# Optimization experiments

Hardware: AMD Instinct MI355X
Metric: run time of the kernel (lower is better)

Reference implementation:

```python
import jax, jax.numpy as jnp
import numpy as np

N_NODES = 50000
N_EDGES = 800000
D_IN = 128
D_OUT = 128


def setup_inputs() -> dict:
    key = jax.random.key(0)
    ks = jax.random.split(key, 10)
    x = jax.random.normal(ks[0], (N_NODES, D_IN), dtype=jnp.float32)
    src = jax.random.randint(ks[1], (N_EDGES,), 0, N_NODES, dtype=jnp.int32)
    dst = jax.random.randint(ks[2], (N_EDGES,), 0, N_NODES, dtype=jnp.int32)
    s = 1.0 / np.sqrt(D_IN)
    def lin(k, din, dout):
        kw, kb = jax.random.split(k)
        W = jax.random.uniform(kw, (din, dout), minval=-s, maxval=s, dtype=jnp.float32)
        b = jax.random.uniform(kb, (dout,), minval=-s, maxval=s, dtype=jnp.float32)
        return W, b
    W1, b1 = lin(ks[3], D_IN, D_IN)
    W2, b2 = lin(ks[4], D_IN, D_IN)
    W3, b3 = lin(ks[5], D_IN, D_OUT)
    return dict(x=x, W1=W1, b1=b1, W2=W2, b2=b2, W3=W3, b3=b3, src=src, dst=dst)


def reference(x, W1, b1, W2, b2, W3, b3, src, dst):
    n = x.shape[0]
    ones = jnp.ones(src.shape[0], dtype=x.dtype)
    in_deg = jax.ops.segment_sum(ones, dst, num_segments=n)    # [N]
    out_deg = jax.ops.segment_sum(ones, src, num_segments=n)   # [N]

    def sage_gcn(h, W, b):
        # DGL SAGEConv(aggregator_type='gcn'), eval mode (feat_drop = identity):
        # h_neigh = (sum_{j in N(i)} h_j + h_i) / (in_deg_i + 1); out = h_neigh @ W + b
        neigh = jax.ops.segment_sum(h[src], dst, num_segments=n)  # [N, D]
        h_neigh = (neigh + h) / (in_deg + 1.0)[:, None]
        return h_neigh @ W + b

    h = sage_gcn(x, W1, b1)
    h = sage_gcn(h, W2, b2)

    # DGL GraphConv norm='both', allow_zero_in_degree=True:
    # out = D_in^{-1/2} A D_out^{-1/2} h W + b, degrees clamped to >= 1
    norm_out = jnp.clip(out_deg, 1.0) ** -0.5
    norm_in = jnp.clip(in_deg, 1.0) ** -0.5
    hs = h * norm_out[:, None]
    agg = jax.ops.segment_sum(hs[src], dst, num_segments=n)
    out = (agg * norm_in[:, None]) @ W3 + b3
    return out
```

## Files before the change

### kernel.cpp

```cpp
#include <hip/hip_runtime.h>

#define NN 50000
#define NE 800000
#define D 128

#define CH 64
#define EPC (NE / CH)
#define RG 8
#define NPR (NN / RG)

typedef short bf16x8 __attribute__((ext_vector_type(8)));
typedef float f32x4 __attribute__((ext_vector_type(4)));


__device__ __forceinline__ unsigned bf16rne(float f) {
  unsigned u = __float_as_uint(f);
  return (u + 0x7fffu + ((u >> 16) & 1u)) >> 16;
}
__device__ __forceinline__ unsigned packbf(float lo, float hi) {
  return bf16rne(lo) | (bf16rne(hi) << 16);
}

__global__ __launch_bounds__(256) void cvt_kernel(const float* __restrict__ x,
                                                  unsigned short* __restrict__ xb, int n4) {
  int i = blockIdx.x * 256 + threadIdx.x;
  if (i < n4) {
    float4 v = ((const float4*)x)[i];
    uint2 p;
    p.x = packbf(v.x, v.y);
    p.y = packbf(v.z, v.w);
    ((uint2*)xb)[i] = p;
  }
}

__global__ __launch_bounds__(256) void wcvt_kernel(const float* __restrict__ W1,
                                                   const float* __restrict__ W2,
                                                   const float* __restrict__ W3,
                                                   unsigned short* __restrict__ T1,
                                                   unsigned short* __restrict__ T2,
                                                   unsigned short* __restrict__ T3) {
  int w = blockIdx.x >> 6;
  int i = (blockIdx.x & 63) * 256 + threadIdx.x;
  const float* W = (w == 0) ? W1 : (w == 1) ? W2 : W3;
  unsigned short* T = (w == 0) ? T1 : (w == 1) ? T2 : T3;
  int n = i >> 7, k = i & 127;
  T[n * 128 + k] = (unsigned short)bf16rne(W[k * 128 + n]);
}

__global__ __launch_bounds__(1024) void hist_kernel(const int* __restrict__ src,
                                                    const int* __restrict__ dst,
                                                    int* __restrict__ partial_dst,
                                                    int* __restrict__ partial_src) {
  __shared__ int hd[NPR];
  __shared__ int hs[NPR];
  int tid = threadIdx.x;
  int c = blockIdx.x >> 3;
  int r = blockIdx.x & 7;
  int base = r * NPR;
  for (int i = tid; i < NPR; i += 1024) { hd[i] = 0; hs[i] = 0; }
  __syncthreads();
  int e0 = c * EPC;
  for (int i = tid; i < EPC; i += 1024) {
    int d = dst[e0 + i];
    int s = src[e0 + i];
    unsigned dr = (unsigned)(d - base);
    unsigned sr = (unsigned)(s - base);
    if (dr < NPR) atomicAdd(&hd[dr], 1);
    if (sr < NPR) atomicAdd(&hs[sr], 1);
  }
  __syncthreads();
  for (int i = tid; i < NPR; i += 1024) {
    partial_dst[c * NN + base + i] = hd[i];
    partial_src[c * NN + base + i] = hs[i];
  }
}

__global__ __launch_bounds__(256) void reduce_kernel(int* __restrict__ partial_dst,
                                                     const int* __restrict__ partial_src,
                                                     int* __restrict__ degtmp,
                                                     int* __restrict__ deg_out, int N) {
  int d = blockIdx.x * 256 + threadIdx.x;
  if (d >= N) return;
  int run = 0;
#pragma unroll
  for (int c = 0; c < CH; ++c) {
    int v = partial_dst[c * NN + d];
    partial_dst[c * NN + d] = run;
    run += v;
  }
  degtmp[d] = run;
  int ro = 0;
#pragma unroll
  for (int c = 0; c < CH; ++c) ro += partial_src[c * NN + d];
  deg_out[d] = ro;
}


__device__ __forceinline__ int block_excl_scan(int v, int* wsum) {
  int lane = threadIdx.x & 63;
  int w = threadIdx.x >> 6;
  int incl = v;
#pragma unroll
  for (int off = 1; off < 64; off <<= 1) {
    int t = __shfl_up(incl, off);
    if (lane >= off) incl += t;
  }
  if (lane == 63) wsum[w] = incl;
  __syncthreads();
  int wo = 0;
#pragma unroll
  for (int j = 0; j < 4; ++j)
    if (j < w) wo += wsum[j];
  return wo + incl - v;
}

__global__ __launch_bounds__(256) void scan1(const int* __restrict__ deg,
                                             int* __restrict__ partials, int N) {
  __shared__ int wsum[4];
  int i = blockIdx.x * 256 + threadIdx.x;
  int v = (i < N) ? deg[i] : 0;
  int excl = block_excl_scan(v, wsum);
  if (threadIdx.x == 255) partials[blockIdx.x] = excl + v;
}

__global__ __launch_bounds__(256) void scan2(int* __restrict__ partials, int nb) {
  __shared__ int wsum[4];
  int v = (threadIdx.x < nb) ? partials[threadIdx.x] : 0;
  int excl = block_excl_scan(v, wsum);
  if (threadIdx.x < nb) partials[threadIdx.x] = excl;
}

__global__ __launch_bounds__(256) void scan3(const int* __restrict__ deg,
                                             const int* __restrict__ partials,
                                             int* __restrict__ row_ptr, int N) {
  __shared__ int wsum[4];
  int i = blockIdx.x * 256 + threadIdx.x;
  int v = (i < N) ? deg[i] : 0;
  int excl = block_excl_scan(v, wsum);
  if (i < N) row_ptr[i] = partials[blockIdx.x] + excl;
  if (blockIdx.x == gridDim.x - 1 && threadIdx.x == 0) row_ptr[N] = NE;
}

__global__ __launch_bounds__(1024) void fill_kernel(const int* __restrict__ src,
                                                    const int* __restrict__ dst,
                                                    const int* __restrict__ row_ptr,
                                                    const int* __restrict__ partial_dst,
                                                    int* __restrict__ csr_src) {
  __shared__ int cur[NPR];
  int tid = threadIdx.x;
  int c = blockIdx.x >> 3;
  int r = blockIdx.x & 7;
  int base = r * NPR;
  for (int i = tid; i < NPR; i += 1024)
    cur[i] = row_ptr[base + i] + partial_dst[c * NN + base + i];
  __syncthreads();
  int e0 = c * EPC;
  for (int i = tid; i < EPC; i += 1024) {
    int d = dst[e0 + i];
    unsigned dr = (unsigned)(d - base);
    if (dr < NPR) {
      int pos = atomicAdd(&cur[dr], 1);
      csr_src[pos] = src[e0 + i];
    }
  }
}

__device__ __forceinline__ void bacc(float* a, uint4 u) {
  a[0] += __uint_as_float(u.x << 16);
  a[1] += __uint_as_float(u.x & 0xffff0000u);
  a[2] += __uint_as_float(u.y << 16);
  a[3] += __uint_as_float(u.y & 0xffff0000u);
  a[4] += __uint_as_float(u.z << 16);
  a[5] += __uint_as_float(u.z & 0xffff0000u);
  a[6] += __uint_as_float(u.w << 16);
  a[7] += __uint_as_float(u.w & 0xffff0000u);
}

template <int MODE>
__global__ __launch_bounds__(256) void agg_kernel(const unsigned short* __restrict__ hb,
                                                  const int* __restrict__ row_ptr,
                                                  const int* __restrict__ csr_src,
                                                  unsigned short* __restrict__ outb, int N) {
  int wid = blockIdx.x * 4 + (threadIdx.x >> 6);
  int lane = threadIdx.x & 63;
  if (wid >= N) return;
  int start = row_ptr[wid];
  int end = row_ptr[wid + 1];
  int q = lane >> 4;
  int col = lane & 15;
  float a0[8] = {0, 0, 0, 0, 0, 0, 0, 0};
  float a1[8] = {0, 0, 0, 0, 0, 0, 0, 0};
  float a2[8] = {0, 0, 0, 0, 0, 0, 0, 0};
  float a3[8] = {0, 0, 0, 0, 0, 0, 0, 0};
  int e = start;
  for (; e + 16 <= end; e += 16) {
    int i0 = csr_src[e + q];
    int i1 = csr_src[e + 4 + q];
    int i2 = csr_src[e + 8 + q];
    int i3 = csr_src[e + 12 + q];
    uint4 u0 = ((const uint4*)(hb + (size_t)i0 * D))[col];
    uint4 u1 = ((const uint4*)(hb + (size_t)i1 * D))[col];
    uint4 u2 = ((const uint4*)(hb + (size_t)i2 * D))[col];
    uint4 u3 = ((const uint4*)(hb + (size_t)i3 * D))[col];
    bacc(a0, u0);
    bacc(a1, u1);
    bacc(a2, u2);
    bacc(a3, u3);
  }
  for (; e + 4 <= end; e += 4) {
    int i0 = csr_src[e + q];
    uint4 u0 = ((const uint4*)(hb + (size_t)i0 * D))[col];
    bacc(a0, u0);
  }
  if (q < end - e) {
    int i0 = csr_src[e + q];
    uint4 u0 = ((const uint4*)(hb + (size_t)i0 * D))[col];
    bacc(a0, u0);
  }
#pragma unroll
  for (int j = 0; j < 8; ++j) a0[j] = (a0[j] + a1[j]) + (a2[j] + a3[j]);
#pragma unroll
  for (int j = 0; j < 8; ++j) {
    a0[j] += __shfl_xor(a0[j], 16);
    a0[j] += __shfl_xor(a0[j], 32);
  }
  int indeg = end - start;
  if (MODE == 0) {
    uint4 s = ((const uint4*)(hb + (size_t)wid * D))[col];
    float sf[8] = {0, 0, 0, 0, 0, 0, 0, 0};
    bacc(sf, s);
    float inv = 1.0f / (float)(indeg + 1);
#pragma unroll
    for (int j = 0; j < 8; ++j) a0[j] = (a0[j] + sf[j]) * inv;
  } else {
    float sc = rsqrtf(fmaxf((float)indeg, 1.0f));
#pragma unroll
    for (int j = 0; j < 8; ++j) a0[j] *= sc;
  }
  if (q == 0) {
    uint4 p;
    p.x = packbf(a0[0], a0[1]);
    p.y = packbf(a0[2], a0[3]);
    p.z = packbf(a0[4], a0[5]);
    p.w = packbf(a0[6], a0[7]);
    ((uint4*)(outb + (size_t)wid * D))[col] = p;
  }
}

template <int MODE, int OUT_BF>
__global__ __launch_bounds__(256) void mgemm_kernel(const unsigned short* __restrict__ A,
                                                    const unsigned short* __restrict__ WT,
                                                    const float* __restrict__ bias,
                                                    const int* __restrict__ deg_out,
                                                    float* __restrict__ outf,
                                                    unsigned short* __restrict__ outb, int N) {
  __shared__ unsigned short sWT[128 * 136];
  int tid = threadIdx.x;
  for (int g = tid; g < 2048; g += 256) {
    int n = g >> 4, c = g & 15;
    uint4 v = ((const uint4*)WT)[g];
    *(uint4*)&sWT[n * 136 + c * 8] = v;
  }
  int wv = tid >> 6;
  int lane = tid & 63;
  int q = lane >> 4;
  int ln = lane & 15;
  int row0 = blockIdx.x * 64 + wv * 16;
  int arow = row0 + ln;
  if (arow >= N) arow = 0;
  const unsigned short* Ar = A + (size_t)arow * 128 + q * 8;
  bf16x8 af0 = *(const bf16x8*)(Ar + 0);
  bf16x8 af1 = *(const bf16x8*)(Ar + 32);
  bf16x8 af2 = *(const bf16x8*)(Ar + 64);
  bf16x8 af3 = *(const bf16x8*)(Ar + 96);
  f32x4 acc[8];
#pragma unroll
  for (int t = 0; t < 8; ++t) acc[t] = (f32x4){0.f, 0.f, 0.f, 0.f};
  __syncthreads();
#pragma unroll
  for (int t = 0; t < 8; ++t) {
    const unsigned short* Wr = &sWT[(t * 16 + ln) * 136 + q * 8];
    bf16x8 b0 = *(const bf16x8*)(Wr + 0);
    bf16x8 b1 = *(const bf16x8*)(Wr + 32);
    bf16x8 b2 = *(const bf16x8*)(Wr + 64);
    bf16x8 b3 = *(const bf16x8*)(Wr + 96);
    acc[t] = __builtin_amdgcn_mfma_f32_16x16x32_bf16(af0, b0, acc[t], 0, 0, 0);
    acc[t] = __builtin_amdgcn_mfma_f32_16x16x32_bf16(af1, b1, acc[t], 0, 0, 0);
    acc[t] = __builtin_amdgcn_mfma_f32_16x16x32_bf16(af2, b2, acc[t], 0, 0, 0);
    acc[t] = __builtin_amdgcn_mfma_f32_16x16x32_bf16(af3, b3, acc[t], 0, 0, 0);
  }
  float scl[4];
#pragma unroll
  for (int r = 0; r < 4; ++r) {
    scl[r] = 1.0f;
    if (MODE == 1) {
      int row = row0 + q * 4 + r;
      int rr = (row < N) ? row : 0;
      scl[r] = rsqrtf(fmaxf((float)deg_out[rr], 1.0f));
    }
  }
#pragma unroll
  for (int t = 0; t < 8; ++t) {
    float b = bias[t * 16 + ln];
#pragma unroll
    for (int r = 0; r < 4; ++r) {
      int row = row0 + q * 4 + r;
      if (row < N) {
        float v = (acc[t][r] + b) * scl[r];
        if (OUT_BF)
          outb[(size_t)row * 128 + t * 16 + ln] = (unsigned short)bf16rne(v);
        else
          outf[(size_t)row * 128 + t * 16 + ln] = v;
      }
    }
  }
}


extern "C" void kernel_launch(void* const* d_in, const int* in_sizes, int n_in,
                              void* d_out, int out_size, void* d_ws, size_t ws_size,
                              hipStream_t stream) {
  const float* x = (const float*)d_in[0];
  const float* W1 = (const float*)d_in[1];
  const float* b1 = (const float*)d_in[2];
  const float* W2 = (const float*)d_in[3];
  const float* b2 = (const float*)d_in[4];
  const float* W3 = (const float*)d_in[5];
  const float* b3 = (const float*)d_in[6];
  const int* src = (const int*)d_in[7];
  const int* dst = (const int*)d_in[8];
  float* out = (float*)d_out;

  const int N = NN, E = NE;

  unsigned short* hbf = (unsigned short*)d_ws;
  unsigned short* aggB = hbf + (size_t)N * D;
  unsigned short* WT1 = aggB + (size_t)N * D;
  unsigned short* WT2 = WT1 + D * D;
  unsigned short* WT3 = WT2 + D * D;
  int* partial_dst = (int*)(WT3 + D * D);
  int* partial_src = partial_dst + (size_t)CH * N;
  int* degtmp = partial_src + (size_t)CH * N;
  int* deg_out = degtmp + N;
  int* row_ptr = deg_out + N;
  int* partials = row_ptr + N + 1;
  int* csr_src = partials + 256;

  const int scanBlocks = (N + 255) / 256;

  cvt_kernel<<<(N * D / 4 + 255) / 256, 256, 0, stream>>>(x, hbf, N * D / 4);
  wcvt_kernel<<<192, 256, 0, stream>>>(W1, W2, W3, WT1, WT2, WT3);
  hist_kernel<<<CH * RG, 1024, 0, stream>>>(src, dst, partial_dst, partial_src);
  reduce_kernel<<<scanBlocks, 256, 0, stream>>>(partial_dst, partial_src, degtmp, deg_out, N);
  scan1<<<scanBlocks, 256, 0, stream>>>(degtmp, partials, N);
  scan2<<<1, 256, 0, stream>>>(partials, scanBlocks);
  scan3<<<scanBlocks, 256, 0, stream>>>(degtmp, partials, row_ptr, N);
  fill_kernel<<<CH * RG, 1024, 0, stream>>>(src, dst, row_ptr, partial_dst, csr_src);

  int aggBlocks = (N + 3) / 4;
  int gemmBlocks = (N + 63) / 64;

  agg_kernel<0><<<aggBlocks, 256, 0, stream>>>(hbf, row_ptr, csr_src, aggB, N);
  mgemm_kernel<0, 1><<<gemmBlocks, 256, 0, stream>>>(aggB, WT1, b1, deg_out, nullptr, hbf, N);
  agg_kernel<0><<<aggBlocks, 256, 0, stream>>>(hbf, row_ptr, csr_src, aggB, N);
  mgemm_kernel<1, 1><<<gemmBlocks, 256, 0, stream>>>(aggB, WT2, b2, deg_out, nullptr, hbf, N);
  agg_kernel<1><<<aggBlocks, 256, 0, stream>>>(hbf, row_ptr, csr_src, aggB, N);
  mgemm_kernel<0, 0><<<gemmBlocks, 256, 0, stream>>>(aggB, WT3, b3, deg_out, out, nullptr, N);
}
```

Measured before the change: 284.8 us.

## Pad CSR rows to multiples of 16 with zero sentinel row, merge prep kernels

Each CSR row is padded to a multiple of 16 entries, and the padding points at an extra all-zero node row. This lets the aggregation loop drop its remainder and tail handling and run only full 16-edge iterations. The conversion kernels are merged into one, and the degree reduction is fused with the first scan pass, which cuts kernel launches. In exchange the gather does extra loads from the zero row (about 7.5 padding entries per node on average). It also needs a new pad kernel and a larger CSR buffer.

```diff
diff --git a/kernel.cpp b/kernel.cpp
--- a/kernel.cpp
+++ b/kernel.cpp
@@ -8,6 +8,7 @@
 #define EPC (NE / CH)
 #define RG 8
 #define NPR (NN / RG)
+#define CSRCAP (NE + 16 * NN)
 
 typedef short bf16x8 __attribute__((ext_vector_type(8)));
 typedef float f32x4 __attribute__((ext_vector_type(4)));
@@ -21,30 +22,34 @@
   return bf16rne(lo) | (bf16rne(hi) << 16);
 }
 
-__global__ __launch_bounds__(256) void cvt_kernel(const float* __restrict__ x,
-                                                  unsigned short* __restrict__ xb, int n4) {
-  int i = blockIdx.x * 256 + threadIdx.x;
-  if (i < n4) {
+__global__ __launch_bounds__(256) void cvtw_kernel(const float* __restrict__ x,
+                                                   const float* __restrict__ W1,
+                                                   const float* __restrict__ W2,
+                                                   const float* __restrict__ W3,
+                                                   unsigned short* __restrict__ hbf,
+                                                   unsigned short* __restrict__ T1,
+                                                   unsigned short* __restrict__ T2,
+                                                   unsigned short* __restrict__ T3) {
+  int b = blockIdx.x;
+  int tid = threadIdx.x;
+  if (b < 6250) {
+    int i = b * 256 + tid;
     float4 v = ((const float4*)x)[i];
     uint2 p;
     p.x = packbf(v.x, v.y);
     p.y = packbf(v.z, v.w);
-    ((uint2*)xb)[i] = p;
-  }
-}
-
-__global__ __launch_bounds__(256) void wcvt_kernel(const float* __restrict__ W1,
-                                                   const float* __restrict__ W2,
-                                                   const float* __restrict__ W3,
-                                                   unsigned short* __restrict__ T1,
-                                                   unsigned short* __restrict__ T2,
-                                                   unsigned short* __restrict__ T3) {
-  int w = blockIdx.x >> 6;
-  int i = (blockIdx.x & 63) * 256 + threadIdx.x;
-  const float* W = (w == 0) ? W1 : (w == 1) ? W2 : W3;
-  unsigned short* T = (w == 0) ? T1 : (w == 1) ? T2 : T3;
-  int n = i >> 7, k = i & 127;
-  T[n * 128 + k] = (unsigned short)bf16rne(W[k * 128 + n]);
+    ((uint2*)hbf)[i] = p;
+  } else if (b < 6442) {
+    int g = b - 6250;
+    int w = g >> 6;
+    int i = (g & 63) * 256 + tid;
+    const float* W = (w == 0) ? W1 : (w == 1) ? W2 : W3;
+    unsigned short* T = (w == 0) ? T1 : (w == 1) ? T2 : T3;
+    int n = i >> 7, k = i & 127;
+    T[n * 128 + k] = (unsigned short)bf16rne(W[k * 128 + n]);
+  } else {
+    if (tid < 16) ((uint4*)(hbf + (size_t)NN * D))[tid] = make_uint4(0, 0, 0, 0);
+  }
 }
 
 __global__ __launch_bounds__(1024) void hist_kernel(const int* __restrict__ src,
@@ -75,27 +80,6 @@
   }
 }
 
-__global__ __launch_bounds__(256) void reduce_kernel(int* __restrict__ partial_dst,
-                                                     const int* __restrict__ partial_src,
-                                                     int* __restrict__ degtmp,
-                                                     int* __restrict__ deg_out, int N) {
-  int d = blockIdx.x * 256 + threadIdx.x;
-  if (d >= N) return;
-  int run = 0;
-#pragma unroll
-  for (int c = 0; c < CH; ++c) {
-    int v = partial_dst[c * NN + d];
-    partial_dst[c * NN + d] = run;
-    run += v;
-  }
-  degtmp[d] = run;
-  int ro = 0;
-#pragma unroll
-  for (int c = 0; c < CH; ++c) ro += partial_src[c * NN + d];
-  deg_out[d] = ro;
-}
-
-
 __device__ __forceinline__ int block_excl_scan(int v, int* wsum) {
   int lane = threadIdx.x & 63;
   int w = threadIdx.x >> 6;
@@ -114,31 +98,47 @@
   return wo + incl - v;
 }
 
-__global__ __launch_bounds__(256) void scan1(const int* __restrict__ deg,
-                                             int* __restrict__ partials, int N) {
+__global__ __launch_bounds__(256) void degscan_kernel(int* __restrict__ partial_dst,
+                                                      const int* __restrict__ partial_src,
+                                                      int* __restrict__ degtmp,
+                                                      int* __restrict__ deg_out,
+                                                      int* __restrict__ row_ptr,
+                                                      int* __restrict__ partials, int N) {
   __shared__ int wsum[4];
-  int i = blockIdx.x * 256 + threadIdx.x;
-  int v = (i < N) ? deg[i] : 0;
-  int excl = block_excl_scan(v, wsum);
-  if (threadIdx.x == 255) partials[blockIdx.x] = excl + v;
-}
-
-__global__ __launch_bounds__(256) void scan2(int* __restrict__ partials, int nb) {
+  int d = blockIdx.x * 256 + threadIdx.x;
+  int run = 0;
+  if (d < N) {
+#pragma unroll
+    for (int c = 0; c < CH; ++c) {
+      int v = partial_dst[c * NN + d];
+      partial_dst[c * NN + d] = run;
+      run += v;
+    }
+    degtmp[d] = run;
+    int ro = 0;
+#pragma unroll
+    for (int c = 0; c < CH; ++c) ro += partial_src[c * NN + d];
+    deg_out[d] = ro;
+  }
+  int pad = (run + 15) & ~15;
+  int excl = block_excl_scan(pad, wsum);
+  if (d < N) row_ptr[d] = excl;
+  if (threadIdx.x == 255) partials[blockIdx.x] = excl + pad;
+}
+
+__global__ __launch_bounds__(256) void scan2(int* __restrict__ partials,
+                                             int* __restrict__ row_ptr, int nb, int N) {
   __shared__ int wsum[4];
   int v = (threadIdx.x < nb) ? partials[threadIdx.x] : 0;
   int excl = block_excl_scan(v, wsum);
   if (threadIdx.x < nb) partials[threadIdx.x] = excl;
-}
-
-__global__ __launch_bounds__(256) void scan3(const int* __restrict__ deg,
-                                             const int* __restrict__ partials,
-                                             int* __restrict__ row_ptr, int N) {
-  __shared__ int wsum[4];
+  if (threadIdx.x == nb - 1) row_ptr[N] = excl + v;
+}
+
+__global__ __launch_bounds__(256) void scan3(int* __restrict__ row_ptr,
+                                             const int* __restrict__ partials, int N) {
   int i = blockIdx.x * 256 + threadIdx.x;
-  int v = (i < N) ? deg[i] : 0;
-  int excl = block_excl_scan(v, wsum);
-  if (i < N) row_ptr[i] = partials[blockIdx.x] + excl;
-  if (blockIdx.x == gridDim.x - 1 && threadIdx.x == 0) row_ptr[N] = NE;
+  if (i < N) row_ptr[i] += partials[blockIdx.x];
 }
 
 __global__ __launch_bounds__(1024) void fill_kernel(const int* __restrict__ src,
@@ -165,6 +165,16 @@
   }
 }
 
+__global__ __launch_bounds__(256) void pad_kernel(const int* __restrict__ row_ptr,
+                                                  const int* __restrict__ degtmp,
+                                                  int* __restrict__ csr_src, int N) {
+  int i = blockIdx.x * 256 + threadIdx.x;
+  if (i >= N) return;
+  int s = row_ptr[i] + degtmp[i];
+  int e = row_ptr[i + 1];
+  for (int j = s; j < e; ++j) csr_src[j] = NN;
+}
+
 __device__ __forceinline__ void bacc(float* a, uint4 u) {
   a[0] += __uint_as_float(u.x << 16);
   a[1] += __uint_as_float(u.x & 0xffff0000u);
@@ -180,24 +190,25 @@
 __global__ __launch_bounds__(256) void agg_kernel(const unsigned short* __restrict__ hb,
                                                   const int* __restrict__ row_ptr,
                                                   const int* __restrict__ csr_src,
+                                                  const int* __restrict__ degtmp,
                                                   unsigned short* __restrict__ outb, int N) {
   int wid = blockIdx.x * 4 + (threadIdx.x >> 6);
   int lane = threadIdx.x & 63;
   if (wid >= N) return;
   int start = row_ptr[wid];
-  int end = row_ptr[wid + 1];
+  int iters = (row_ptr[wid + 1] - start) >> 4;
   int q = lane >> 4;
   int col = lane & 15;
   float a0[8] = {0, 0, 0, 0, 0, 0, 0, 0};
   float a1[8] = {0, 0, 0, 0, 0, 0, 0, 0};
   float a2[8] = {0, 0, 0, 0, 0, 0, 0, 0};
   float a3[8] = {0, 0, 0, 0, 0, 0, 0, 0};
-  int e = start;
-  for (; e + 16 <= end; e += 16) {
-    int i0 = csr_src[e + q];
-    int i1 = csr_src[e + 4 + q];
-    int i2 = csr_src[e + 8 + q];
-    int i3 = csr_src[e + 12 + q];
+  const int* ce = csr_src + start + q;
+  for (int it = 0; it < iters; ++it, ce += 16) {
+    int i0 = ce[0];
+    int i1 = ce[4];
+    int i2 = ce[8];
+    int i3 = ce[12];
     uint4 u0 = ((const uint4*)(hb + (size_t)i0 * D))[col];
     uint4 u1 = ((const uint4*)(hb + (size_t)i1 * D))[col];
     uint4 u2 = ((const uint4*)(hb + (size_t)i2 * D))[col];
@@ -207,16 +218,6 @@
     bacc(a2, u2);
     bacc(a3, u3);
   }
-  for (; e + 4 <= end; e += 4) {
-    int i0 = csr_src[e + q];
-    uint4 u0 = ((const uint4*)(hb + (size_t)i0 * D))[col];
-    bacc(a0, u0);
-  }
-  if (q < end - e) {
-    int i0 = csr_src[e + q];
-    uint4 u0 = ((const uint4*)(hb + (size_t)i0 * D))[col];
-    bacc(a0, u0);
-  }
 #pragma unroll
   for (int j = 0; j < 8; ++j) a0[j] = (a0[j] + a1[j]) + (a2[j] + a3[j]);
 #pragma unroll
@@ -224,7 +225,7 @@
     a0[j] += __shfl_xor(a0[j], 16);
     a0[j] += __shfl_xor(a0[j], 32);
   }
-  int indeg = end - start;
+  int indeg = degtmp[wid];
   if (MODE == 0) {
     uint4 s = ((const uint4*)(hb + (size_t)wid * D))[col];
     float sf[8] = {0, 0, 0, 0, 0, 0, 0, 0};
@@ -331,39 +332,39 @@
   const int* dst = (const int*)d_in[8];
   float* out = (float*)d_out;
 
-  const int N = NN, E = NE;
+  const int N = NN;
 
   unsigned short* hbf = (unsigned short*)d_ws;
-  unsigned short* aggB = hbf + (size_t)N * D;
-  unsigned short* WT1 = aggB + (size_t)N * D;
+  unsigned short* aggB = hbf + (size_t)(NN + 1) * D;
+  unsigned short* WT1 = aggB + (size_t)NN * D;
   unsigned short* WT2 = WT1 + D * D;
   unsigned short* WT3 = WT2 + D * D;
   int* partial_dst = (int*)(WT3 + D * D);
-  int* partial_src = partial_dst + (size_t)CH * N;
-  int* degtmp = partial_src + (size_t)CH * N;
-  int* deg_out = degtmp + N;
-  int* row_ptr = deg_out + N;
-  int* partials = row_ptr + N + 1;
+  int* partial_src = partial_dst + (size_t)CH * NN;
+  int* degtmp = partial_src + (size_t)CH * NN;
+  int* deg_out = degtmp + NN;
+  int* row_ptr = deg_out + NN;
+  int* partials = row_ptr + NN + 1;
   int* csr_src = partials + 256;
 
   const int scanBlocks = (N + 255) / 256;
 
-  cvt_kernel<<<(N * D / 4 + 255) / 256, 256, 0, stream>>>(x, hbf, N * D / 4);
-  wcvt_kernel<<<192, 256, 0, stream>>>(W1, W2, W3, WT1, WT2, WT3);
+  cvtw_kernel<<<6443, 256, 0, stream>>>(x, W1, W2, W3, hbf, WT1, WT2, WT3);
   hist_kernel<<<CH * RG, 1024, 0, stream>>>(src, dst, partial_dst, partial_src);
-  reduce_kernel<<<scanBlocks, 256, 0, stream>>>(partial_dst, partial_src, degtmp, deg_out, N);
-  scan1<<<scanBlocks, 256, 0, stream>>>(degtmp, partials, N);
-  scan2<<<1, 256, 0, stream>>>(partials, scanBlocks);
-  scan3<<<scanBlocks, 256, 0, stream>>>(degtmp, partials, row_ptr, N);
+  degscan_kernel<<<scanBlocks, 256, 0, stream>>>(partial_dst, partial_src, degtmp,
+                                                 deg_out, row_ptr, partials, N);
+  scan2<<<1, 256, 0, stream>>>(partials, row_ptr, scanBlocks, N);
+  scan3<<<scanBlocks, 256, 0, stream>>>(row_ptr, partials, N);
   fill_kernel<<<CH * RG, 1024, 0, stream>>>(src, dst, row_ptr, partial_dst, csr_src);
+  pad_kernel<<<scanBlocks, 256, 0, stream>>>(row_ptr, degtmp, csr_src, N);
 
   int aggBlocks = (N + 3) / 4;
   int gemmBlocks = (N + 63) / 64;
 
-  agg_kernel<0><<<aggBlocks, 256, 0, stream>>>(hbf, row_ptr, csr_src, aggB, N);
+  agg_kernel<0><<<aggBlocks, 256, 0, stream>>>(hbf, row_ptr, csr_src, degtmp, aggB, N);
   mgemm_kernel<0, 1><<<gemmBlocks, 256, 0, stream>>>(aggB, WT1, b1, deg_out, nullptr, hbf, N);
-  agg_kernel<0><<<aggBlocks, 256, 0, stream>>>(hbf, row_ptr, csr_src, aggB, N);
+  agg_kernel<0><<<aggBlocks, 256, 0, stream>>>(hbf, row_ptr, csr_src, degtmp, aggB, N);
   mgemm_kernel<1, 1><<<gemmBlocks, 256, 0, stream>>>(aggB, WT2, b2, deg_out, nullptr, hbf, N);
-  agg_kernel<1><<<aggBlocks, 256, 0, stream>>>(hbf, row_ptr, csr_src, aggB, N);
+  agg_kernel<1><<<aggBlocks, 256, 0, stream>>>(hbf, row_ptr, csr_src, degtmp, aggB, N);
   mgemm_kernel<0, 0><<<gemmBlocks, 256, 0, stream>>>(aggB, WT3, b3, deg_out, out, nullptr, N);
 }
```

Result: faster. 273.0 us (-4.1%).
